# Kernel optimization log

Hardware: AMD Instinct MI355X
Metric: run time of the kernel (lower is better)

Reference implementation:

```python
import jax, jax.numpy as jnp
import numpy as np
import math

FANO_LINES = [(0,1,2),(0,3,4),(0,6,5),(1,3,5),(1,4,6),(2,3,6),(2,5,4)]
WINDOW = 16

def fano_mask(T: int) -> jnp.ndarray:
    """[7,T,T] bool mask: head h attends to j if (j%7 in line_h and j<=i) or i-WINDOW<=j<=i."""
    membership = np.zeros((7, 7), dtype=bool)
    for h, line in enumerate(FANO_LINES):
        membership[h, list(line)] = True
    j = np.arange(T)
    fano = membership[:, j % 7]                      # [7,T]
    i = j[:, None]
    causal = (j[None, :] <= i)                       # [T,T]
    local = causal & (j[None, :] >= i - WINDOW)      # [T,T]
    mask = (fano[:, None, :] & causal[None]) | local[None]
    return jnp.asarray(mask)

def setup_inputs() -> dict:
    key = jax.random.key(0)
    ks = jax.random.split(key, 5)
    B, T, D = 1, 4096, 896
    s = 1.0 / math.sqrt(D)
    return {
        "x":  jax.random.normal(ks[0], (B, T, D), dtype=jnp.float32),
        "Wq": jax.random.normal(ks[1], (D, D), dtype=jnp.float32) * s,
        "Wk": jax.random.normal(ks[2], (D, D), dtype=jnp.float32) * s,
        "Wv": jax.random.normal(ks[3], (D, D), dtype=jnp.float32) * s,
        "Wo": jax.random.normal(ks[4], (D, D), dtype=jnp.float32) * s,
    }

def reference(x, Wq, Wk, Wv, Wo):
    B, T, D = x.shape
    H = 7
    hd = D // H
    # torch Linear: x @ W.T
    q = (x @ Wq.T).reshape(B, T, H, hd)
    k = (x @ Wk.T).reshape(B, T, H, hd)
    v = (x @ Wv.T).reshape(B, T, H, hd)
    scale = 1.0 / math.sqrt(hd)
    scores = jnp.einsum('bthc,bshc->bhts', q, k) * scale   # [B,7,T,T]
    mask = fano_mask(T)                                    # [7,T,T]
    neg = jnp.asarray(-jnp.inf, dtype=scores.dtype)
    scores = jnp.where(mask[None], scores, neg)
    attn = jax.nn.softmax(scores, axis=-1)
    out = jnp.einsum('bhts,bshc->bthc', attn, v).reshape(B, T, D)
    return out @ Wo.T
```

## Files before the change

kernel.cpp:

```cpp
#include <hip/hip_runtime.h>
#include <stdint.h>

typedef unsigned short ushort_t;
typedef __bf16 bf16x8 __attribute__((ext_vector_type(8)));
typedef float f32x4 __attribute__((ext_vector_type(4)));

#define T_SEQ 4096
#define D_MODEL 896
#define CHUNKS_PER_BLOCK 4
#define MAXSPLIT 8

#define LSK 136
#define LSV 72
#define LSP 72

__constant__ int d_LINEMASK[7] = {0x07, 0x19, 0x61, 0x2A, 0x52, 0x4C, 0x34};
__constant__ int d_R[7][3] = {{0,1,2},{0,3,4},{0,5,6},{1,3,5},{1,4,6},{2,3,6},{2,4,5}};

__device__ inline unsigned f2bf(float f) {
    unsigned x = __float_as_uint(f);
    return (x + 0x7fffu + ((x >> 16) & 1u)) >> 16;
}
__device__ inline float lo_f(unsigned x) { return __uint_as_float(x << 16); }
__device__ inline float hi_f(unsigned x) { return __uint_as_float(x & 0xFFFF0000u); }

__host__ __device__ inline int nsplit_of(int t) {
    int a = (192 * t + 189) / 7 + 3;
    int nch_ub = (a + 63) >> 6;
    return (nch_ub + 2 + CHUNKS_PER_BLOCK - 1) / CHUNKS_PER_BLOCK;
}

__global__ __launch_bounds__(256)
void cvt5(const float* __restrict__ x,  const float* __restrict__ wq,
          const float* __restrict__ wk, const float* __restrict__ wv,
          const float* __restrict__ wo,
          ushort_t* __restrict__ xb,  ushort_t* __restrict__ wqb,
          ushort_t* __restrict__ wkb, ushort_t* __restrict__ wvb,
          ushort_t* __restrict__ wob) {
    const int ten = blockIdx.y;
    const float* s = (ten == 0) ? x : (ten == 1) ? wq : (ten == 2) ? wk
                   : (ten == 3) ? wv : wo;
    ushort_t* d = (ten == 0) ? xb : (ten == 1) ? wqb : (ten == 2) ? wkb
                : (ten == 3) ? wvb : wob;
    const int n8 = ((ten == 0) ? T_SEQ * D_MODEL : D_MODEL * D_MODEL) >> 3;
    for (int i = blockIdx.x * 256 + threadIdx.x; i < n8; i += gridDim.x * 256) {
        float4 a = ((const float4*)s)[2 * i];
        float4 b = ((const float4*)s)[2 * i + 1];
        uint4 u;
        u.x = f2bf(a.x) | (f2bf(a.y) << 16);
        u.y = f2bf(a.z) | (f2bf(a.w) << 16);
        u.z = f2bf(b.x) | (f2bf(b.y) << 16);
        u.w = f2bf(b.z) | (f2bf(b.w) << 16);
        ((uint4*)d)[i] = u;
    }
}

__device__ __forceinline__ void async_cp16(const void* g, void* l) {
    __builtin_amdgcn_global_load_lds(
        (__attribute__((address_space(1))) void*)g,
        (__attribute__((address_space(3))) void*)l,
        16, 0, 0);
}

template <bool C32>
__global__ __launch_bounds__(256)
void gemm_nt_dma(const ushort_t* __restrict__ A,
                 const ushort_t* __restrict__ B0,
                 const ushort_t* __restrict__ B1,
                 const ushort_t* __restrict__ B2,
                 void* __restrict__ C0,
                 void* __restrict__ C1,
                 void* __restrict__ C2) {
    const int z = blockIdx.z;
    const ushort_t* B = (z == 0) ? B0 : (z == 1) ? B1 : B2;
    void* C = (z == 0) ? C0 : (z == 1) ? C1 : C2;

    const int K = D_MODEL, N = D_MODEL;
    const int i0 = blockIdx.x * 128;
    const int n0 = blockIdx.y * 128;

    __shared__ __align__(16) ushort_t As[128 * 32];
    __shared__ __align__(16) ushort_t Bs[128 * 32];

    const int t = threadIdx.x;
    const int w = t >> 6, lane = t & 63;
    const int wm = (w >> 1) * 64, wn = (w & 1) * 64;
    const int lr = lane & 15, lq = lane >> 4;

    const int srow = w * 16 + (lane >> 2);
    const int scol = (lane & 3) * 8;
    const ushort_t* gA0 = A + (size_t)(i0 + srow) * K + scol;
    const ushort_t* gA1 = A + (size_t)(i0 + 64 + srow) * K + scol;
    const ushort_t* gB0 = B + (size_t)(n0 + srow) * K + scol;
    const ushort_t* gB1 = B + (size_t)(n0 + 64 + srow) * K + scol;
    ushort_t* lA0 = &As[(w * 16) * 32];
    ushort_t* lA1 = &As[(64 + w * 16) * 32];
    ushort_t* lB0 = &Bs[(w * 16) * 32];
    ushort_t* lB1 = &Bs[(64 + w * 16) * 32];

    f32x4 acc[4][4];
#pragma unroll
    for (int a = 0; a < 4; a++)
#pragma unroll
        for (int b = 0; b < 4; b++) acc[a][b] = (f32x4){0.f, 0.f, 0.f, 0.f};

    for (int k0 = 0; k0 < K; k0 += 32) {
        __syncthreads();
        async_cp16(gA0 + k0, lA0);
        async_cp16(gA1 + k0, lA1);
        async_cp16(gB0 + k0, lB0);
        async_cp16(gB1 + k0, lB1);
        __builtin_amdgcn_s_waitcnt(0);
        __syncthreads();

        bf16x8 af[4], bfr[4];
#pragma unroll
        for (int mi = 0; mi < 4; mi++)
            af[mi] = *(const bf16x8*)&As[(wm + mi * 16 + lr) * 32 + lq * 8];
#pragma unroll
        for (int ni = 0; ni < 4; ni++)
            bfr[ni] = *(const bf16x8*)&Bs[(wn + ni * 16 + lr) * 32 + lq * 8];
#pragma unroll
        for (int mi = 0; mi < 4; mi++)
#pragma unroll
            for (int ni = 0; ni < 4; ni++)
                acc[mi][ni] = __builtin_amdgcn_mfma_f32_16x16x32_bf16(
                    af[mi], bfr[ni], acc[mi][ni], 0, 0, 0);
    }

    if (C32) {
        float* Cf = (float*)C;
#pragma unroll
        for (int mi = 0; mi < 4; mi++)
#pragma unroll
            for (int ni = 0; ni < 4; ni++)
#pragma unroll
                for (int r = 0; r < 4; r++) {
                    int row = i0 + wm + mi * 16 + lq * 4 + r;
                    int col = n0 + wn + ni * 16 + lr;
                    Cf[(size_t)row * N + col] = acc[mi][ni][r];
                }
    } else {
        ushort_t* Cb = (ushort_t*)C;
#pragma unroll
        for (int mi = 0; mi < 4; mi++)
#pragma unroll
            for (int ni = 0; ni < 4; ni++)
#pragma unroll
                for (int r = 0; r < 4; r++) {
                    int row = i0 + wm + mi * 16 + lq * 4 + r;
                    int col = n0 + wn + ni * 16 + lr;
                    Cb[(size_t)row * N + col] = (ushort_t)f2bf(acc[mi][ni][r]);
                }
    }
}

__device__ inline void vt_scatter8(ushort_t* vtcol, uint4 vv) {
    vtcol[0 * LSV] = (ushort_t)(vv.x & 0xFFFFu);
    vtcol[1 * LSV] = (ushort_t)(vv.x >> 16);
    vtcol[2 * LSV] = (ushort_t)(vv.y & 0xFFFFu);
    vtcol[3 * LSV] = (ushort_t)(vv.y >> 16);
    vtcol[4 * LSV] = (ushort_t)(vv.z & 0xFFFFu);
    vtcol[5 * LSV] = (ushort_t)(vv.z >> 16);
    vtcol[6 * LSV] = (ushort_t)(vv.w & 0xFFFFu);
    vtcol[7 * LSV] = (ushort_t)(vv.w >> 16);
}

__device__ inline int jof(int p, int r0, int r1, int r2) {
    int g = p / 3, rs = p - 3 * g;
    return 7 * g + ((rs == 0) ? r0 : (rs == 1) ? r1 : r2);
}

__device__ __forceinline__ void issue_kv(const ushort_t* __restrict__ Kb,
                                         const ushort_t* __restrict__ Vb,
                                         int j, int h, int dim0,
                                         uint4 kreg[4], uint4 vreg[4]) {
    if (j >= 0 && j < T_SEQ) {
        const ushort_t* kp = Kb + (size_t)j * D_MODEL + h * 128 + dim0;
        const ushort_t* vp = Vb + (size_t)j * D_MODEL + h * 128 + dim0;
#pragma unroll
        for (int v = 0; v < 4; v++) {
            kreg[v] = *(const uint4*)(kp + v * 8);
            vreg[v] = *(const uint4*)(vp + v * 8);
        }
    } else {
        uint4 zz = {0u, 0u, 0u, 0u};
#pragma unroll
        for (int v = 0; v < 4; v++) { kreg[v] = zz; vreg[v] = zz; }
    }
}

__device__ __forceinline__ void write_kv(ushort_t* Ks, ushort_t* Vt,
                                         int kk, int dim0,
                                         const uint4 kreg[4], const uint4 vreg[4]) {
#pragma unroll
    for (int v = 0; v < 4; v++) {
        *(uint4*)&Ks[kk * LSK + dim0 + v * 8] = kreg[v];
        vt_scatter8(&Vt[(dim0 + v * 8) * LSV + kk], vreg[v]);
    }
}

__global__ __launch_bounds__(256, 3)
void fano_attn_split(const ushort_t* __restrict__ Qb,
                     const ushort_t* __restrict__ Kb,
                     const ushort_t* __restrict__ Vb,
                     ushort_t* __restrict__ Opart,
                     float* __restrict__ Lm) {
    const int h = blockIdx.y;
    const int p = (int)gridDim.x - 1 - (int)blockIdx.x;

    int tile = 63, pbase0 = 0;
    for (int u = 0; u < 64; ++u) {
        int s = nsplit_of(u);
        if (p < pbase0 + s) { tile = u; break; }
        pbase0 += s;
    }
    const int sp = p - pbase0;
    const int Sloc = nsplit_of(tile);

    const int i0 = tile * 64;
    const int t = threadIdx.x;
    const int w = t >> 6, lane = t & 63;
    const int lr = lane & 15, quad = lane >> 4;
    const int iw0 = i0 + w * 16;

    __shared__ __align__(16) ushort_t Ks[64 * LSK];
    __shared__ __align__(16) ushort_t Vt[128 * LSV];
    __shared__ __align__(16) ushort_t Ps[64 * LSP];

    const int lm = d_LINEMASK[h];
    const int r0 = d_R[h][0], r1 = d_R[h][1], r2 = d_R[h][2];
    const float scale = 0.08838834764831845f;

    bf16x8 qf[4];
    {
        const ushort_t* qrow = Qb + (size_t)(iw0 + lr) * D_MODEL + h * 128;
#pragma unroll
        for (int f = 0; f < 4; f++)
            qf[f] = *(const bf16x8*)(qrow + f * 32 + quad * 8);
    }

    f32x4 O[8];
#pragma unroll
    for (int dt = 0; dt < 8; dt++) O[dt] = (f32x4){0.f, 0.f, 0.f, 0.f};
    float m[4] = {-1e30f, -1e30f, -1e30f, -1e30f};
    float l[4] = {0.f, 0.f, 0.f, 0.f};

    const int imax = i0 + 63;
    const int ncomp = (imax - r0) / 7 + (imax - r1) / 7 + (imax - r2) / 7 + 3;
    const int nch = (ncomp + 63) >> 6;
    const int ntot = nch + 2;
    const int cstart = (sp * ntot) / Sloc;
    const int cend = ((sp + 1) * ntot) / Sloc;

    auto chunk_j = [&](int cc) -> int {
        if (cc >= nch) {
            const int jbase = (cc == nch) ? i0 - 16 : i0 + 48;
            return jbase + lane;
        }
        return jof(cc * 64 + lane, r0, r1, r2);
    };

    uint4 kreg[4], vreg[4];
    if (cstart < cend)
        issue_kv(Kb, Vb, chunk_j(cstart), h, w * 32, kreg, vreg);

    for (int cc = cstart; cc < cend; cc++) {
        const bool band = (cc >= nch);
        const int jbase = (cc == nch) ? i0 - 16 : i0 + 48;

        __syncthreads();
        write_kv(Ks, Vt, lane, w * 32, kreg, vreg);
        __syncthreads();

        if (cc + 1 < cend)
            issue_kv(Kb, Vb, chunk_j(cc + 1), h, w * 32, kreg, vreg);

        {
            int jmin = band ? jbase : jof(cc * 64, r0, r1, r2);
            if (jmin > iw0 + 15) continue;
        }

        f32x4 S[4];
#pragma unroll
        for (int tn = 0; tn < 4; tn++) S[tn] = (f32x4){0.f, 0.f, 0.f, 0.f};
#pragma unroll
        for (int f = 0; f < 4; f++) {
            bf16x8 kf[4];
#pragma unroll
            for (int tn = 0; tn < 4; tn++)
                kf[tn] = *(const bf16x8*)&Ks[(tn * 16 + lr) * LSK + f * 32 + quad * 8];
#pragma unroll
            for (int tn = 0; tn < 4; tn++)
                S[tn] = __builtin_amdgcn_mfma_f32_16x16x32_bf16(qf[f], kf[tn], S[tn], 0, 0, 0);
        }

#pragma unroll
        for (int tn = 0; tn < 4; tn++) {
            int j;
            bool okl = true;
            if (band) {
                j = jbase + tn * 16 + lr;
                int jm = ((j % 7) + 7) % 7;
                okl = (j >= 0) && !((lm >> jm) & 1);
            } else {
                j = jof(cc * 64 + tn * 16 + lr, r0, r1, r2);
            }
#pragma unroll
            for (int r = 0; r < 4; r++) {
                int ir = iw0 + quad * 4 + r;
                bool ok = okl && (j <= ir) && (!band || j >= ir - 16);
                S[tn][r] = ok ? S[tn][r] * scale : -1e30f;
            }
        }

        float a4[4], pvv[4][4];
#pragma unroll
        for (int r = 0; r < 4; r++) {
            float cm = fmaxf(fmaxf(S[0][r], S[1][r]), fmaxf(S[2][r], S[3][r]));
            cm = fmaxf(cm, __shfl_xor(cm, 1));
            cm = fmaxf(cm, __shfl_xor(cm, 2));
            cm = fmaxf(cm, __shfl_xor(cm, 4));
            cm = fmaxf(cm, __shfl_xor(cm, 8));
            float mn = fmaxf(fmaxf(m[r], cm), -60.f);
            a4[r] = __expf(m[r] - mn);
            m[r] = mn;
            float rs_ = 0.f;
#pragma unroll
            for (int tn = 0; tn < 4; tn++) {
                pvv[tn][r] = __expf(S[tn][r] - mn);
                rs_ += pvv[tn][r];
            }
            rs_ += __shfl_xor(rs_, 1);
            rs_ += __shfl_xor(rs_, 2);
            rs_ += __shfl_xor(rs_, 4);
            rs_ += __shfl_xor(rs_, 8);
            l[r] = l[r] * a4[r] + rs_;
            ushort_t* pp = &Ps[(w * 16 + quad * 4 + r) * LSP + lr];
            pp[0]  = (ushort_t)f2bf(pvv[0][r]);
            pp[16] = (ushort_t)f2bf(pvv[1][r]);
            pp[32] = (ushort_t)f2bf(pvv[2][r]);
            pp[48] = (ushort_t)f2bf(pvv[3][r]);
        }
#pragma unroll
        for (int dt = 0; dt < 8; dt++)
#pragma unroll
            for (int r = 0; r < 4; r++) O[dt][r] *= a4[r];

        bf16x8 pf0 = *(const bf16x8*)&Ps[(w * 16 + lr) * LSP + quad * 8];
        bf16x8 pf1 = *(const bf16x8*)&Ps[(w * 16 + lr) * LSP + 32 + quad * 8];
#pragma unroll
        for (int dt = 0; dt < 8; dt++) {
            bf16x8 v0 = *(const bf16x8*)&Vt[(dt * 16 + lr) * LSV + quad * 8];
            bf16x8 v1 = *(const bf16x8*)&Vt[(dt * 16 + lr) * LSV + 32 + quad * 8];
            O[dt] = __builtin_amdgcn_mfma_f32_16x16x32_bf16(pf0, v0, O[dt], 0, 0, 0);
            O[dt] = __builtin_amdgcn_mfma_f32_16x16x32_bf16(pf1, v1, O[dt], 0, 0, 0);
        }
    }

    const size_t pbase = ((size_t)p * 7 + h) * 64;
#pragma unroll
    for (int dt = 0; dt < 8; dt++)
#pragma unroll
        for (int r = 0; r < 4; r++) {
            int lrow = w * 16 + quad * 4 + r;
            Opart[(pbase + lrow) * 128 + dt * 16 + lr] = (ushort_t)f2bf(O[dt][r]);
        }
    if (lr == 0) {
#pragma unroll
        for (int r = 0; r < 4; r++) {
            int lrow = w * 16 + quad * 4 + r;
            Lm[(pbase + lrow) * 2 + 0] = m[r];
            Lm[(pbase + lrow) * 2 + 1] = l[r];
        }
    }
}

__global__ __launch_bounds__(256)
void attn_merge(const ushort_t* __restrict__ Opart,
                const float* __restrict__ Lm,
                ushort_t* __restrict__ Ab) {
    const int h = blockIdx.y;
    const int tt = blockIdx.x;
    int pb = 0;
    for (int u = 0; u < tt; ++u) pb += nsplit_of(u);
    const int S = nsplit_of(tt);
    const int lrow = threadIdx.x >> 2;
    const int row = tt * 64 + lrow;
    const int d0 = (threadIdx.x & 3) * 32;

    float ms[MAXSPLIT], ls[MAXSPLIT], M = -1e30f;
#pragma unroll
    for (int s = 0; s < MAXSPLIT; s++) {
        ms[s] = -1e30f;
        ls[s] = 0.f;
        if (s < S) {
            size_t q = (((size_t)(pb + s) * 7 + h) * 64 + lrow) * 2;
            ms[s] = Lm[q];
            ls[s] = Lm[q + 1];
        }
        M = fmaxf(M, ms[s]);
    }
    float L = 0.f, c[MAXSPLIT];
#pragma unroll
    for (int s = 0; s < MAXSPLIT; s++) {
        c[s] = __expf(ms[s] - M);
        L += c[s] * ls[s];
    }
    float acc[32];
#pragma unroll
    for (int k = 0; k < 32; k++) acc[k] = 0.f;
#pragma unroll
    for (int s = 0; s < MAXSPLIT; s++) {
        if (s < S) {
            const float cs = c[s];
            const ushort_t* op =
                Opart + (((size_t)(pb + s) * 7 + h) * 64 + lrow) * 128 + d0;
#pragma unroll
            for (int v = 0; v < 4; v++) {
                uint4 u = *(const uint4*)(op + v * 8);
                acc[v * 8 + 0] += cs * lo_f(u.x);
                acc[v * 8 + 1] += cs * hi_f(u.x);
                acc[v * 8 + 2] += cs * lo_f(u.y);
                acc[v * 8 + 3] += cs * hi_f(u.y);
                acc[v * 8 + 4] += cs * lo_f(u.z);
                acc[v * 8 + 5] += cs * hi_f(u.z);
                acc[v * 8 + 6] += cs * lo_f(u.w);
                acc[v * 8 + 7] += cs * hi_f(u.w);
            }
        }
    }
    float invL = 1.f / L;
    ushort_t* dst = Ab + (size_t)row * D_MODEL + h * 128 + d0;
#pragma unroll
    for (int v = 0; v < 4; v++) {
        uint4 u;
        u.x = f2bf(acc[v * 8 + 0] * invL) | (f2bf(acc[v * 8 + 1] * invL) << 16);
        u.y = f2bf(acc[v * 8 + 2] * invL) | (f2bf(acc[v * 8 + 3] * invL) << 16);
        u.z = f2bf(acc[v * 8 + 4] * invL) | (f2bf(acc[v * 8 + 5] * invL) << 16);
        u.w = f2bf(acc[v * 8 + 6] * invL) | (f2bf(acc[v * 8 + 7] * invL) << 16);
        *(uint4*)(dst + v * 8) = u;
    }
}

extern "C" void kernel_launch(void* const* d_in, const int* in_sizes, int n_in,
                              void* d_out, int out_size, void* d_ws, size_t ws_size,
                              hipStream_t stream) {
    const float* x  = (const float*)d_in[0];
    const float* Wq = (const float*)d_in[1];
    const float* Wk = (const float*)d_in[2];
    const float* Wv = (const float*)d_in[3];
    const float* Wo = (const float*)d_in[4];

    int NP = 0;
    for (int u = 0; u < 64; ++u) NP += nsplit_of(u);

    const size_t n  = (size_t)T_SEQ * D_MODEL;
    const size_t nw = (size_t)D_MODEL * D_MODEL;
    ushort_t* xb  = (ushort_t*)d_ws + 128;
    ushort_t* Wqb = xb + n;
    ushort_t* Wkb = Wqb + nw;
    ushort_t* Wvb = Wkb + nw;
    ushort_t* Wob = Wvb + nw;
    ushort_t* Qb  = Wob + nw;
    ushort_t* Kb  = Qb + n;
    ushort_t* Vb  = Kb + n;
    ushort_t* Ab  = Vb + n;
    ushort_t* Opart = Ab + n;
    float*    Lm  = (float*)(Opart + (size_t)NP * 7 * 64 * 128);

    cvt5<<<dim3(1792, 5), 256, 0, stream>>>(x, Wq, Wk, Wv, Wo,
                                            xb, Wqb, Wkb, Wvb, Wob);
    gemm_nt_dma<false><<<dim3(32, 7, 3), 256, 0, stream>>>(
        xb, Wqb, Wkb, Wvb, Qb, Kb, Vb);
    fano_attn_split<<<dim3(NP, 7), 256, 0, stream>>>(
        Qb, Kb, Vb, Opart, Lm);
    attn_merge<<<dim3(64, 7), 256, 0, stream>>>(Opart, Lm, Ab);
    gemm_nt_dma<true><<<dim3(32, 7, 1), 256, 0, stream>>>(
        Ab, Wob, Wob, Wob, d_out, d_out, d_out);
}
```

Baseline: 139.0 us.

## Transpose QK MFMA to keep softmax per-lane and pass P via shuffles

Swaps the MFMA operand order so each lane holds a full query row's scores. This lets the softmax max and sum reductions run across the four quads with two shuffles instead of four per row. The probability tile is repacked into the PV operand layout with cross-lane shuffles instead of a round trip through the Ps shared-memory buffer. Dropping that buffer cuts LDS use, and launch bounds are raised to 4 blocks per SM. In exchange the code does extra shuffles and selects, and the added register pressure at higher occupancy could cause spills.

Result: no change. 138.7 us (-0.2%).

```diff
diff --git a/kernel.cpp b/kernel.cpp
--- a/kernel.cpp
+++ b/kernel.cpp
@@ -12,7 +12,6 @@
 
 #define LSK 136
 #define LSV 72
-#define LSP 72
 
 __constant__ int d_LINEMASK[7] = {0x07, 0x19, 0x61, 0x2A, 0x52, 0x4C, 0x34};
 __constant__ int d_R[7][3] = {{0,1,2},{0,3,4},{0,5,6},{1,3,5},{1,4,6},{2,3,6},{2,4,5}};
@@ -200,7 +199,7 @@
     }
 }
 
-__global__ __launch_bounds__(256, 3)
+__global__ __launch_bounds__(256, 4)
 void fano_attn_split(const ushort_t* __restrict__ Qb,
                      const ushort_t* __restrict__ Kb,
                      const ushort_t* __restrict__ Vb,
@@ -226,7 +225,6 @@
 
     __shared__ __align__(16) ushort_t Ks[64 * LSK];
     __shared__ __align__(16) ushort_t Vt[128 * LSV];
-    __shared__ __align__(16) ushort_t Ps[64 * LSP];
 
     const int lm = d_LINEMASK[h];
     const int r0 = d_R[h][0], r1 = d_R[h][1], r2 = d_R[h][2];
@@ -243,8 +241,8 @@
     f32x4 O[8];
 #pragma unroll
     for (int dt = 0; dt < 8; dt++) O[dt] = (f32x4){0.f, 0.f, 0.f, 0.f};
-    float m[4] = {-1e30f, -1e30f, -1e30f, -1e30f};
-    float l[4] = {0.f, 0.f, 0.f, 0.f};
+    float m = -1e30f;
+    float l = 0.f;
 
     const int imax = i0 + 63;
     const int ncomp = (imax - r0) / 7 + (imax - r1) / 7 + (imax - r2) / 7 + 3;
@@ -265,6 +263,8 @@
     if (cstart < cend)
         issue_kv(Kb, Vb, chunk_j(cstart), h, w * 32, kreg, vreg);
 
+    const int iq = iw0 + lr;
+
     for (int cc = cstart; cc < cend; cc++) {
         const bool band = (cc >= nch);
         const int jbase = (cc == nch) ? i0 - 16 : i0 + 48;
@@ -292,63 +292,96 @@
                 kf[tn] = *(const bf16x8*)&Ks[(tn * 16 + lr) * LSK + f * 32 + quad * 8];
 #pragma unroll
             for (int tn = 0; tn < 4; tn++)
-                S[tn] = __builtin_amdgcn_mfma_f32_16x16x32_bf16(qf[f], kf[tn], S[tn], 0, 0, 0);
+                S[tn] = __builtin_amdgcn_mfma_f32_16x16x32_bf16(kf[tn], qf[f], S[tn], 0, 0, 0);
         }
 
 #pragma unroll
         for (int tn = 0; tn < 4; tn++) {
-            int j;
-            bool okl = true;
             if (band) {
-                j = jbase + tn * 16 + lr;
-                int jm = ((j % 7) + 7) % 7;
-                okl = (j >= 0) && !((lm >> jm) & 1);
+#pragma unroll
+                for (int r = 0; r < 4; r++) {
+                    int j = jbase + tn * 16 + quad * 4 + r;
+                    int jm = ((j % 7) + 7) % 7;
+                    bool ok = (j >= 0) && !((lm >> jm) & 1) &&
+                              (j <= iq) && (j >= iq - 16);
+                    S[tn][r] = ok ? S[tn][r] * scale : -1e30f;
+                }
             } else {
-                j = jof(cc * 64 + tn * 16 + lr, r0, r1, r2);
+                int p0 = cc * 64 + tn * 16 + quad * 4;
+                int g = p0 / 3, rs = p0 - 3 * g;
+#pragma unroll
+                for (int r = 0; r < 4; r++) {
+                    int j = 7 * g + ((rs == 0) ? r0 : (rs == 1) ? r1 : r2);
+                    S[tn][r] = (j <= iq) ? S[tn][r] * scale : -1e30f;
+                    if (++rs == 3) { rs = 0; ++g; }
+                }
             }
+        }
+
+        float cm = -1e30f;
+#pragma unroll
+        for (int tn = 0; tn < 4; tn++)
+#pragma unroll
+            for (int r = 0; r < 4; r++) cm = fmaxf(cm, S[tn][r]);
+        cm = fmaxf(cm, __shfl_xor(cm, 16));
+        cm = fmaxf(cm, __shfl_xor(cm, 32));
+        float mn = fmaxf(fmaxf(m, cm), -60.f);
+        float a = __expf(m - mn);
+        m = mn;
+        float pr[4][4];
+        float rs_ = 0.f;
+#pragma unroll
+        for (int tn = 0; tn < 4; tn++)
 #pragma unroll
             for (int r = 0; r < 4; r++) {
-                int ir = iw0 + quad * 4 + r;
-                bool ok = okl && (j <= ir) && (!band || j >= ir - 16);
-                S[tn][r] = ok ? S[tn][r] * scale : -1e30f;
+                pr[tn][r] = __expf(S[tn][r] - mn);
+                rs_ += pr[tn][r];
             }
-        }
-
-        float a4[4], pvv[4][4];
-#pragma unroll
-        for (int r = 0; r < 4; r++) {
-            float cm = fmaxf(fmaxf(S[0][r], S[1][r]), fmaxf(S[2][r], S[3][r]));
-            cm = fmaxf(cm, __shfl_xor(cm, 1));
-            cm = fmaxf(cm, __shfl_xor(cm, 2));
-            cm = fmaxf(cm, __shfl_xor(cm, 4));
-            cm = fmaxf(cm, __shfl_xor(cm, 8));
-            float mn = fmaxf(fmaxf(m[r], cm), -60.f);
-            a4[r] = __expf(m[r] - mn);
-            m[r] = mn;
-            float rs_ = 0.f;
-#pragma unroll
-            for (int tn = 0; tn < 4; tn++) {
-                pvv[tn][r] = __expf(S[tn][r] - mn);
-                rs_ += pvv[tn][r];
-            }
-            rs_ += __shfl_xor(rs_, 1);
-            rs_ += __shfl_xor(rs_, 2);
-            rs_ += __shfl_xor(rs_, 4);
-            rs_ += __shfl_xor(rs_, 8);
-            l[r] = l[r] * a4[r] + rs_;
-            ushort_t* pp = &Ps[(w * 16 + quad * 4 + r) * LSP + lr];
-            pp[0]  = (ushort_t)f2bf(pvv[0][r]);
-            pp[16] = (ushort_t)f2bf(pvv[1][r]);
-            pp[32] = (ushort_t)f2bf(pvv[2][r]);
-            pp[48] = (ushort_t)f2bf(pvv[3][r]);
-        }
+        rs_ += __shfl_xor(rs_, 16);
+        rs_ += __shfl_xor(rs_, 32);
+        l = l * a + rs_;
+
+        float a4[4];
+#pragma unroll
+        for (int r = 0; r < 4; r++) a4[r] = __shfl(a, quad * 4 + r);
 #pragma unroll
         for (int dt = 0; dt < 8; dt++)
 #pragma unroll
             for (int r = 0; r < 4; r++) O[dt][r] *= a4[r];
 
-        bf16x8 pf0 = *(const bf16x8*)&Ps[(w * 16 + lr) * LSP + quad * 8];
-        bf16x8 pf1 = *(const bf16x8*)&Ps[(w * 16 + lr) * LSP + 32 + quad * 8];
+        unsigned u01[4], u23[4];
+#pragma unroll
+        for (int tn = 0; tn < 4; tn++) {
+            u01[tn] = f2bf(pr[tn][0]) | (f2bf(pr[tn][1]) << 16);
+            u23[tn] = f2bf(pr[tn][2]) | (f2bf(pr[tn][3]) << 16);
+        }
+        const int srcA = 32 * (quad & 1) + lr;
+        const int srcB = srcA + 16;
+        const bool hi = (quad >= 2);
+        uint4 t0, t1;
+        {
+            unsigned d0a = __shfl(u01[0], srcA), d0b = __shfl(u01[1], srcA);
+            unsigned d1a = __shfl(u23[0], srcA), d1b = __shfl(u23[1], srcA);
+            unsigned d2a = __shfl(u01[0], srcB), d2b = __shfl(u01[1], srcB);
+            unsigned d3a = __shfl(u23[0], srcB), d3b = __shfl(u23[1], srcB);
+            t0.x = hi ? d0b : d0a;
+            t0.y = hi ? d1b : d1a;
+            t0.z = hi ? d2b : d2a;
+            t0.w = hi ? d3b : d3a;
+        }
+        {
+            unsigned d0a = __shfl(u01[2], srcA), d0b = __shfl(u01[3], srcA);
+            unsigned d1a = __shfl(u23[2], srcA), d1b = __shfl(u23[3], srcA);
+            unsigned d2a = __shfl(u01[2], srcB), d2b = __shfl(u01[3], srcB);
+            unsigned d3a = __shfl(u23[2], srcB), d3b = __shfl(u23[3], srcB);
+            t1.x = hi ? d0b : d0a;
+            t1.y = hi ? d1b : d1a;
+            t1.z = hi ? d2b : d2a;
+            t1.w = hi ? d3b : d3a;
+        }
+        bf16x8 pf0 = *(const bf16x8*)&t0;
+        bf16x8 pf1 = *(const bf16x8*)&t1;
+
 #pragma unroll
         for (int dt = 0; dt < 8; dt++) {
             bf16x8 v0 = *(const bf16x8*)&Vt[(dt * 16 + lr) * LSV + quad * 8];
@@ -366,13 +399,10 @@
             int lrow = w * 16 + quad * 4 + r;
             Opart[(pbase + lrow) * 128 + dt * 16 + lr] = (ushort_t)f2bf(O[dt][r]);
         }
-    if (lr == 0) {
-#pragma unroll
-        for (int r = 0; r < 4; r++) {
-            int lrow = w * 16 + quad * 4 + r;
-            Lm[(pbase + lrow) * 2 + 0] = m[r];
-            Lm[(pbase + lrow) * 2 + 1] = l[r];
-        }
+    if (quad == 0) {
+        int lrow = w * 16 + lr;
+        Lm[(pbase + lrow) * 2 + 0] = m;
+        Lm[(pbase + lrow) * 2 + 1] = l;
     }
 }
 
```
